# Performance work log

Hardware: AMD Instinct MI355X
Metric: run time of the kernel (lower is better)

Reference implementation:

```python
import jax, jax.numpy as jnp
import numpy as np

B, S, D, H, DH = 2, 4096, 768, 12, 64

def setup_inputs() -> dict:
    key = jax.random.key(0)
    kx, kq, kk, kv = jax.random.split(key, 4)
    x = jax.random.normal(kx, (B, S, D), dtype=jnp.float32)
    # per-head Q/K/V projection weights, stacked over heads: [H, d_in, d_out]
    Wq = jax.random.normal(kq, (H, D, DH), dtype=jnp.float32) * 0.02
    Wk = jax.random.normal(kk, (H, D, DH), dtype=jnp.float32) * 0.02
    Wv = jax.random.normal(kv, (H, D, DH), dtype=jnp.float32) * 0.02
    return {"x": x, "Wq": Wq, "Wk": Wk, "Wv": Wv}

def reference(x, Wq, Wk, Wv):
    b, s, _ = x.shape
    # per-head linear projections (qkv_bias=False), batched over heads
    q = jnp.einsum('bsd,hde->bhse', x, Wq)  # [B,H,S,DH]
    k = jnp.einsum('bsd,hde->bhse', x, Wk)
    v = jnp.einsum('bsd,hde->bhse', x, Wv)
    scale = 1.0 / jnp.sqrt(jnp.asarray(q.shape[-1], q.dtype))
    scores = jnp.einsum('bhqe,bhke->bhqk', q, k) * scale  # [B,H,S,S]
    causal_mask = jnp.triu(jnp.ones((s, s), dtype=bool), k=1)
    scores = jnp.where(causal_mask, -jnp.inf, scores)
    attn = jax.nn.softmax(scores, axis=-1)  # dropout p=0 -> identity
    ctx = jnp.einsum('bhqk,bhke->bhqe', attn, v)  # [B,H,S,DH]
    # concat heads on last dim (matches torch.cat of per-head outputs)
    return ctx.transpose(0, 2, 1, 3).reshape(b, s, -1)  # [B,S,H*DH]
```

## Files before the change

### kernel.cpp

```cpp
#include <hip/hip_runtime.h>
#include <hip/hip_bf16.h>
#include <stdint.h>

#define B_  2
#define S_  4096
#define D_  768
#define H_  12
#define DH_ 64
#define BS_ (B_*S_)

typedef __bf16 bf16x8 __attribute__((ext_vector_type(8)));
typedef short  svec8  __attribute__((ext_vector_type(8)));
typedef float  fvec4  __attribute__((ext_vector_type(4)));
typedef int    ivec4  __attribute__((ext_vector_type(4)));
typedef unsigned short ushort_t;

__device__ __forceinline__ ushort_t bfc(float f){
    return __builtin_bit_cast(ushort_t, (__bf16)f);
}

__device__ __forceinline__ unsigned cvt_pk_bf16(float lo, float hi){
    unsigned r;
    asm("v_cvt_pk_bf16_f32 %0, %1, %2" : "=v"(r) : "v"(lo), "v"(hi));
    return r;
}

__device__ __forceinline__ fvec4 mfma16(svec8 a, svec8 b, fvec4 c){
    return __builtin_amdgcn_mfma_f32_16x16x32_bf16(
        __builtin_bit_cast(bf16x8, a), __builtin_bit_cast(bf16x8, b), c, 0, 0, 0);
}

__global__ __launch_bounds__(256) void prep(
    const float* __restrict__ X,
    const float* __restrict__ Wq, const float* __restrict__ Wk, const float* __restrict__ Wv,
    ushort_t* __restrict__ Xb, ushort_t* __restrict__ Wsz)
{
    const int bid = blockIdx.x;
    if (bid < 3072) {
        size_t idx = ((size_t)bid * 256 + threadIdx.x) * 8;
        float4 d0 = *(const float4*)(X + idx);
        float4 d1 = *(const float4*)(X + idx + 4);
        bf16x8 pk;
        pk[0] = (__bf16)d0.x; pk[1] = (__bf16)d0.y;
        pk[2] = (__bf16)d0.z; pk[3] = (__bf16)d0.w;
        pk[4] = (__bf16)d1.x; pk[5] = (__bf16)d1.y;
        pk[6] = (__bf16)d1.z; pk[7] = (__bf16)d1.w;
        *(svec8*)(Xb + idx) = __builtin_bit_cast(svec8, pk);
    } else {
        const int v  = bid - 3072;
        const int wt = v % 3;
        const int hk = v / 3;
        const int h  = hk / 12, kt = hk % 12;
        const float* W  = (wt == 0) ? Wq : (wt == 1) ? Wk : Wv;
        const float* Wh = W + (size_t)h * (D_ * DH_) + (size_t)kt * 64 * DH_;
        ushort_t* dst = Wsz + (size_t)(hk * 3 + wt) * 4096;
        #pragma unroll
        for (int i = 0; i < 2; i++) {
            int a    = (threadIdx.x + 256 * i) * 8;
            int k5   = a >> 11;
            int nblk = (a >> 9) & 3;
            int n    = nblk * 16 + ((a >> 5) & 15);
            int q2   = (a >> 3) & 3;
            int k0   = k5 * 32 + q2 * 8;
            bf16x8 pk;
            #pragma unroll
            for (int j = 0; j < 8; j++) pk[j] = (__bf16)Wh[(k0 + j) * DH_ + n];
            *(svec8*)(dst + a) = __builtin_bit_cast(svec8, pk);
        }
    }
}

__global__ __launch_bounds__(256, 3) void qkv_proj(
    const ushort_t* __restrict__ Xb, const ushort_t* __restrict__ Wsz,
    ushort_t* __restrict__ Qb, ushort_t* __restrict__ Kb, ushort_t* __restrict__ Vg)
{
    const int m0 = blockIdx.x * 128;
    const int h  = blockIdx.y;

    __shared__ ushort_t smem[128 * 64 + 3 * 4096];
    ushort_t* Xs  = smem;
    ushort_t* Wts = smem + 128 * 64;
    ushort_t* XsT = smem;

    const int tid  = threadIdx.x;
    const int w    = tid >> 6;
    const int lane = tid & 63;
    const int quad = lane >> 4;
    const int l15  = lane & 15;
    const int lp8  = (l15 * 4 + quad) * 8;

    fvec4 acc[3][2][4];
    #pragma unroll
    for (int wt = 0; wt < 3; wt++)
        #pragma unroll
        for (int i = 0; i < 2; i++)
            #pragma unroll
            for (int j = 0; j < 4; j++) acc[wt][i][j] = (fvec4){0.f, 0.f, 0.f, 0.f};

    const ushort_t* xsrc = Xb + (size_t)m0 * D_;
    const ushort_t* wsrc = Wsz + (size_t)(h * 12) * 3 * 4096;

    int xr[4], xdu[4];
    #pragma unroll
    for (int i = 0; i < 4; i++) {
        int v = tid + 256 * i;
        int r = v >> 3, t = v & 7;
        xr[i]  = r * D_ + t * 8;
        xdu[i] = (((r >> 4) * 2 + (t >> 2)) * 64 + (r & 15) * 4 + (t & 3)) * 8;
    }

    svec8 xd[4];
    #pragma unroll
    for (int i = 0; i < 4; i++) xd[i] = *(const svec8*)(xsrc + xr[i]);

    for (int kt = 0; kt < 12; kt++) {
        const ushort_t* wp = wsrc + (size_t)kt * 3 * 4096;
        svec8 wd[6];
        #pragma unroll
        for (int j = 0; j < 6; j++)
            wd[j] = *(const svec8*)(wp + (tid + 256 * j) * 8);
        #pragma unroll
        for (int i = 0; i < 4; i++) *(svec8*)(Xs + xdu[i]) = xd[i];
        #pragma unroll
        for (int j = 0; j < 6; j++) *(svec8*)(Wts + (tid + 256 * j) * 8) = wd[j];
        __syncthreads();

        if (kt < 11) {
            #pragma unroll
            for (int i = 0; i < 4; i++)
                xd[i] = *(const svec8*)(xsrc + xr[i] + (kt + 1) * 64);
        }

        #pragma unroll
        for (int ks = 0; ks < 2; ks++) {
            svec8 a0 = *(const svec8*)(Xs + (4 * w + ks) * 512 + lp8);
            svec8 a1 = *(const svec8*)(Xs + (4 * w + 2 + ks) * 512 + lp8);
            #pragma unroll
            for (int wt = 0; wt < 3; wt++)
                #pragma unroll
                for (int ns = 0; ns < 4; ns++) {
                    svec8 b = *(const svec8*)(Wts + (wt * 8 + ks * 4 + ns) * 512 + lp8);
                    acc[wt][0][ns] = mfma16(a0, b, acc[wt][0][ns]);
                    acc[wt][1][ns] = mfma16(a1, b, acc[wt][1][ns]);
                }
        }
        __syncthreads();
    }

    const float qs = 0.18033688011112042f;
    #pragma unroll
    for (int ms = 0; ms < 2; ms++)
        #pragma unroll
        for (int ns = 0; ns < 4; ns++)
            #pragma unroll
            for (int r = 0; r < 4; r++) {
                int row = m0 + 32 * w + ms * 16 + quad * 4 + r;
                int col = h * DH_ + ns * 16 + l15;
                Qb[(size_t)row * D_ + col] = bfc(acc[0][ms][ns][r] * qs);
                Kb[(size_t)row * D_ + col] = bfc(acc[1][ms][ns][r]);
            }
    #pragma unroll
    for (int ms = 0; ms < 2; ms++)
        #pragma unroll
        for (int ns = 0; ns < 4; ns++)
            #pragma unroll
            for (int r = 0; r < 4; r++) {
                int sl = 32 * w + ms * 16 + quad * 4 + r;
                int e  = ns * 16 + l15;
                XsT[e * 136 + sl] = bfc(acc[2][ms][ns][r]);
            }
    __syncthreads();
    #pragma unroll
    for (int i = 0; i < 4; i++) {
        int v = tid + 256 * i;
        int e = v >> 4, s0 = (v & 15) * 8;
        svec8 d = *(const svec8*)(XsT + e * 136 + s0);
        *(svec8*)(Vg + (size_t)(h * DH_ + e) * BS_ + m0 + s0) = d;
    }
}

__global__ __launch_bounds__(256, 3) void attn(
    const ushort_t* __restrict__ Qb, const ushort_t* __restrict__ Kb,
    const ushort_t* __restrict__ Vg, float* __restrict__ Out)
{
    const int fid = blockIdx.x;
    const int c   = fid & 255;
    const int rnd = fid >> 8;
    const int t   = c & 31;
    const int u   = c >> 5;
    const int qtp = (rnd == 0) ? t : (rnd == 1) ? ((t + 16) & 31)
                                                : (t < 16 ? 30 - 2 * t : 63 - 2 * t);
    const int hb  = rnd * 8 + u;
    const int h   = hb % H_;
    const int b   = hb / H_;
    const int q0  = qtp * 128;
    const int qt2 = 2 * qtp + 1;

    const int tid  = threadIdx.x;
    const int w    = tid >> 6;
    const int lane = tid & 63;
    const int quad = lane >> 4;
    const int l15  = lane & 15;

    __shared__ ushort_t Ks[64 * 72];
    __shared__ ushort_t Vt[64 * 72];

    const size_t hboff = (size_t)b * S_ * D_ + (size_t)h * DH_;
    const ushort_t* Vh = Vg + (size_t)h * DH_ * BS_ + (size_t)b * S_;

    const int sr = tid >> 3;
    const int sc = (tid & 7) * 8;
    const int pr0 = (((sr      >> 2) & 1) << 5) | (((sr      >> 5) & 1) << 4) |
                    (((sr      >> 4) & 1) << 3) | (((sr      >> 3) & 1) << 2) | (sr & 3);
    const int sr1 = sr + 32;
    const int pr1 = (((sr1 >> 2) & 1) << 5) | (((sr1 >> 5) & 1) << 4) |
                    (((sr1 >> 4) & 1) << 3) | (((sr1 >> 3) & 1) << 2) | (sr1 & 3);

    svec8 aqA[2], aqB[2];
    {
        const ushort_t* qra = Qb + hboff + (size_t)(q0 + 16 * w + l15) * D_;
        aqA[0] = *(const svec8*)(qra + quad * 8);
        aqA[1] = *(const svec8*)(qra + 32 + quad * 8);
        const ushort_t* qrb = qra + (size_t)64 * D_;
        aqB[0] = *(const svec8*)(qrb + quad * 8);
        aqB[1] = *(const svec8*)(qrb + 32 + quad * 8);
    }

    float miA = -INFINITY, miB = -INFINITY;
    float lsA = 0.f, lsB = 0.f;
    fvec4 accA[4], accB[4];
    #pragma unroll
    for (int n = 0; n < 4; n++) {
        accA[n] = (fvec4){0.f, 0.f, 0.f, 0.f};
        accB[n] = (fvec4){0.f, 0.f, 0.f, 0.f};
    }

    const ushort_t* kp = Kb + hboff + (size_t)sr * D_ + sc;
    const ushort_t* vp = Vh + (size_t)sr * BS_ + sc;

    svec8 kd[2], vd[2];
    kd[0] = *(const svec8*)(kp);
    kd[1] = *(const svec8*)(kp + (size_t)32 * D_);
    vd[0] = *(const svec8*)(vp);
    vd[1] = *(const svec8*)(vp + (size_t)32 * BS_);
    kp += (size_t)64 * D_;
    vp += 64;
    *(svec8*)(Ks + pr0 * 72 + sc) = kd[0];
    *(svec8*)(Ks + pr1 * 72 + sc) = kd[1];
    *(svec8*)(Vt + sr  * 72 + sc) = vd[0];
    *(svec8*)(Vt + sr1 * 72 + sc) = vd[1];

    for (int kt = 0; kt <= qt2; ++kt) {
        __syncthreads();

        if (kt < qt2) {
            kd[0] = *(const svec8*)(kp);
            kd[1] = *(const svec8*)(kp + (size_t)32 * D_);
            vd[0] = *(const svec8*)(vp);
            vd[1] = *(const svec8*)(vp + (size_t)32 * BS_);
            kp += (size_t)64 * D_;
            vp += 64;
        }

        fvec4 stA[4], stB[4];
        #pragma unroll
        for (int n = 0; n < 4; n++) {
            stA[n] = (fvec4){0.f, 0.f, 0.f, 0.f};
            stB[n] = (fvec4){0.f, 0.f, 0.f, 0.f};
        }
        #pragma unroll
        for (int ks = 0; ks < 2; ks++)
            #pragma unroll
            for (int n = 0; n < 4; n++) {
                svec8 ka = *(const svec8*)(Ks + (n * 16 + l15) * 72 + ks * 32 + quad * 8);
                stA[n] = mfma16(ka, aqA[ks], stA[n]);
                stB[n] = mfma16(ka, aqB[ks], stB[n]);
            }

        if (kt == qt2 - 1) {
            #pragma unroll
            for (int n = 0; n < 4; n++)
                #pragma unroll
                for (int r = 0; r < 4; r++) {
                    int key = (n & 1) * 32 + quad * 8 + (n >> 1) * 4 + r;
                    int row = 16 * w + l15;
                    if (key > row) stA[n][r] = -INFINITY;
                }
        }
        if (kt == qt2) {
            #pragma unroll
            for (int n = 0; n < 4; n++)
                #pragma unroll
                for (int r = 0; r < 4; r++) {
                    stA[n][r] = -INFINITY;
                    int key = (n & 1) * 32 + quad * 8 + (n >> 1) * 4 + r;
                    int row = 16 * w + l15;
                    if (key > row) stB[n][r] = -INFINITY;
                }
        }

        float mxA, mxB;
        {
            float m1 = fmaxf(fmaxf(stA[0][0], stA[0][1]), stA[0][2]);
            m1 = fmaxf(fmaxf(m1, stA[0][3]), stA[1][0]);
            m1 = fmaxf(fmaxf(m1, stA[1][1]), stA[1][2]);
            m1 = fmaxf(m1, stA[1][3]);
            float m2 = fmaxf(fmaxf(stA[2][0], stA[2][1]), stA[2][2]);
            m2 = fmaxf(fmaxf(m2, stA[2][3]), stA[3][0]);
            m2 = fmaxf(fmaxf(m2, stA[3][1]), stA[3][2]);
            m2 = fmaxf(m2, stA[3][3]);
            mxA = fmaxf(m1, m2);
            mxA = fmaxf(mxA, __shfl_xor(mxA, 16));
            mxA = fmaxf(mxA, __shfl_xor(mxA, 32));
        }
        {
            float m1 = fmaxf(fmaxf(stB[0][0], stB[0][1]), stB[0][2]);
            m1 = fmaxf(fmaxf(m1, stB[0][3]), stB[1][0]);
            m1 = fmaxf(fmaxf(m1, stB[1][1]), stB[1][2]);
            m1 = fmaxf(m1, stB[1][3]);
            float m2 = fmaxf(fmaxf(stB[2][0], stB[2][1]), stB[2][2]);
            m2 = fmaxf(fmaxf(m2, stB[2][3]), stB[3][0]);
            m2 = fmaxf(fmaxf(m2, stB[3][1]), stB[3][2]);
            m2 = fmaxf(m2, stB[3][3]);
            mxB = fmaxf(m1, m2);
            mxB = fmaxf(mxB, __shfl_xor(mxB, 16));
            mxB = fmaxf(mxB, __shfl_xor(mxB, 32));
        }

        if (__any((mxA > miA) || (mxB > miB))) {
            float mnA = fmaxf(miA, mxA), mnB = fmaxf(miB, mxB);
            float aA = exp2f(miA - mnA), aB = exp2f(miB - mnB);
            miA = mnA; miB = mnB;
            lsA *= aA; lsB *= aB;
            #pragma unroll
            for (int r = 0; r < 4; r++) {
                float arA = __shfl(aA, quad * 16 + quad * 4 + r);
                float arB = __shfl(aB, quad * 16 + quad * 4 + r);
                #pragma unroll
                for (int n = 0; n < 4; n++) {
                    accA[n][r] *= arA;
                    accB[n][r] *= arB;
                }
            }
        }

        svec8 apA0, apA1, apB0, apB1;
        {
            ivec4 ai0, ai1;
            float ps[4];
            #pragma unroll
            for (int n = 0; n < 4; n++) {
                float p0 = exp2f(stA[n][0] - miA);
                float p1 = exp2f(stA[n][1] - miA);
                float p2 = exp2f(stA[n][2] - miA);
                float p3 = exp2f(stA[n][3] - miA);
                ps[n] = (p0 + p1) + (p2 + p3);
                unsigned d0 = cvt_pk_bf16(p0, p1);
                unsigned d1 = cvt_pk_bf16(p2, p3);
                if (n == 0)      { ai0[0] = (int)d0; ai0[1] = (int)d1; }
                else if (n == 1) { ai1[0] = (int)d0; ai1[1] = (int)d1; }
                else if (n == 2) { ai0[2] = (int)d0; ai0[3] = (int)d1; }
                else             { ai1[2] = (int)d0; ai1[3] = (int)d1; }
            }
            lsA += (ps[0] + ps[2]) + (ps[1] + ps[3]);
            apA0 = __builtin_bit_cast(svec8, ai0);
            apA1 = __builtin_bit_cast(svec8, ai1);
        }
        {
            ivec4 ai0, ai1;
            float ps[4];
            #pragma unroll
            for (int n = 0; n < 4; n++) {
                float p0 = exp2f(stB[n][0] - miB);
                float p1 = exp2f(stB[n][1] - miB);
                float p2 = exp2f(stB[n][2] - miB);
                float p3 = exp2f(stB[n][3] - miB);
                ps[n] = (p0 + p1) + (p2 + p3);
                unsigned d0 = cvt_pk_bf16(p0, p1);
                unsigned d1 = cvt_pk_bf16(p2, p3);
                if (n == 0)      { ai0[0] = (int)d0; ai0[1] = (int)d1; }
                else if (n == 1) { ai1[0] = (int)d0; ai1[1] = (int)d1; }
                else if (n == 2) { ai0[2] = (int)d0; ai0[3] = (int)d1; }
                else             { ai1[2] = (int)d0; ai1[3] = (int)d1; }
            }
            lsB += (ps[0] + ps[2]) + (ps[1] + ps[3]);
            apB0 = __builtin_bit_cast(svec8, ai0);
            apB1 = __builtin_bit_cast(svec8, ai1);
        }

        #pragma unroll
        for (int ks = 0; ks < 2; ks++) {
            svec8 apa = ks ? apA1 : apA0;
            svec8 apb = ks ? apB1 : apB0;
            #pragma unroll
            for (int n = 0; n < 4; n++) {
                svec8 bv = *(const svec8*)(Vt + (n * 16 + l15) * 72 + ks * 32 + quad * 8);
                accA[n] = mfma16(apa, bv, accA[n]);
                accB[n] = mfma16(apb, bv, accB[n]);
            }
        }

        __syncthreads();

        if (kt < qt2) {
            *(svec8*)(Ks + pr0 * 72 + sc) = kd[0];
            *(svec8*)(Ks + pr1 * 72 + sc) = kd[1];
            *(svec8*)(Vt + sr  * 72 + sc) = vd[0];
            *(svec8*)(Vt + sr1 * 72 + sc) = vd[1];
        }
    }

    float lsumA = lsA;
    lsumA += __shfl_xor(lsumA, 16);
    lsumA += __shfl_xor(lsumA, 32);
    float lsumB = lsB;
    lsumB += __shfl_xor(lsumB, 16);
    lsumB += __shfl_xor(lsumB, 32);
    #pragma unroll
    for (int r = 0; r < 4; r++) {
        float liA = __shfl(lsumA, quad * 16 + quad * 4 + r);
        float liB = __shfl(lsumB, quad * 16 + quad * 4 + r);
        int rowA = q0 + 16 * w + quad * 4 + r;
        #pragma unroll
        for (int n = 0; n < 4; n++) {
            int col = h * DH_ + n * 16 + l15;
            Out[((size_t)b * S_ + rowA) * D_ + col]      = accA[n][r] / liA;
            Out[((size_t)b * S_ + rowA + 64) * D_ + col] = accB[n][r] / liB;
        }
    }
}

extern "C" void kernel_launch(void* const* d_in, const int* in_sizes, int n_in,
                              void* d_out, int out_size, void* d_ws, size_t ws_size,
                              hipStream_t stream)
{
    const float* X  = (const float*)d_in[0];
    const float* Wq = (const float*)d_in[1];
    const float* Wk = (const float*)d_in[2];
    const float* Wv = (const float*)d_in[3];

    ushort_t* Qb = (ushort_t*)d_ws;
    ushort_t* Kb = Qb + (size_t)BS_ * D_;
    ushort_t* Vg = Kb + (size_t)BS_ * D_;

    ushort_t* Xb  = (ushort_t*)d_out;
    ushort_t* Wsz = Xb + (size_t)BS_ * D_;
    float* Out = (float*)d_out;

    prep<<<dim3(3072 + 432), dim3(256), 0, stream>>>(X, Wq, Wk, Wv, Xb, Wsz);
    qkv_proj<<<dim3(64, H_), dim3(256), 0, stream>>>(Xb, Wsz, Qb, Kb, Vg);
    attn<<<dim3(768), dim3(256), 0, stream>>>(Qb, Kb, Vg, Out);
}
```

Before: 248.6 us.

## Shrink attention blocks to 64-row tiles and read projection weights directly from global

The attention kernel now runs 128-thread blocks, each covering a 64-row query tile with two waves of 32 rows. Tiles are scheduled longest-first, and the paired-tile balancing scheme plus the two-step diagonal masking are replaced by a single diagonal step. This gives a finer grid for load balance and occupancy, at the cost of each K/V tile being reused by fewer query rows. The QKV projection also stops staging the pre-swizzled weights in LDS and loads MFMA B operands straight from global memory, which shrinks shared memory but adds global/L2 traffic inside the inner loop.

```diff
diff --git a/kernel.cpp b/kernel.cpp
--- a/kernel.cpp
+++ b/kernel.cpp
@@ -77,9 +77,8 @@
     const int m0 = blockIdx.x * 128;
     const int h  = blockIdx.y;
 
-    __shared__ ushort_t smem[128 * 64 + 3 * 4096];
+    __shared__ ushort_t smem[64 * 136];
     ushort_t* Xs  = smem;
-    ushort_t* Wts = smem + 128 * 64;
     ushort_t* XsT = smem;
 
     const int tid  = threadIdx.x;
@@ -98,7 +97,7 @@
             for (int j = 0; j < 4; j++) acc[wt][i][j] = (fvec4){0.f, 0.f, 0.f, 0.f};
 
     const ushort_t* xsrc = Xb + (size_t)m0 * D_;
-    const ushort_t* wsrc = Wsz + (size_t)(h * 12) * 3 * 4096;
+    const ushort_t* wsrc = Wsz + (size_t)(h * 12) * 3 * 4096 + lp8;
 
     int xr[4], xdu[4];
     #pragma unroll
@@ -114,15 +113,8 @@
     for (int i = 0; i < 4; i++) xd[i] = *(const svec8*)(xsrc + xr[i]);
 
     for (int kt = 0; kt < 12; kt++) {
-        const ushort_t* wp = wsrc + (size_t)kt * 3 * 4096;
-        svec8 wd[6];
-        #pragma unroll
-        for (int j = 0; j < 6; j++)
-            wd[j] = *(const svec8*)(wp + (tid + 256 * j) * 8);
         #pragma unroll
         for (int i = 0; i < 4; i++) *(svec8*)(Xs + xdu[i]) = xd[i];
-        #pragma unroll
-        for (int j = 0; j < 6; j++) *(svec8*)(Wts + (tid + 256 * j) * 8) = wd[j];
         __syncthreads();
 
         if (kt < 11) {
@@ -131,18 +123,23 @@
                 xd[i] = *(const svec8*)(xsrc + xr[i] + (kt + 1) * 64);
         }
 
+        const ushort_t* wp = wsrc + (size_t)kt * 3 * 4096;
         #pragma unroll
         for (int ks = 0; ks < 2; ks++) {
             svec8 a0 = *(const svec8*)(Xs + (4 * w + ks) * 512 + lp8);
             svec8 a1 = *(const svec8*)(Xs + (4 * w + 2 + ks) * 512 + lp8);
             #pragma unroll
-            for (int wt = 0; wt < 3; wt++)
+            for (int wt = 0; wt < 3; wt++) {
+                svec8 wb[4];
+                #pragma unroll
+                for (int ns = 0; ns < 4; ns++)
+                    wb[ns] = *(const svec8*)(wp + (wt * 8 + ks * 4 + ns) * 512);
                 #pragma unroll
                 for (int ns = 0; ns < 4; ns++) {
-                    svec8 b = *(const svec8*)(Wts + (wt * 8 + ks * 4 + ns) * 512 + lp8);
-                    acc[wt][0][ns] = mfma16(a0, b, acc[wt][0][ns]);
-                    acc[wt][1][ns] = mfma16(a1, b, acc[wt][1][ns]);
+                    acc[wt][0][ns] = mfma16(a0, wb[ns], acc[wt][0][ns]);
+                    acc[wt][1][ns] = mfma16(a1, wb[ns], acc[wt][1][ns]);
                 }
+            }
         }
         __syncthreads();
     }
@@ -179,22 +176,16 @@
     }
 }
 
-__global__ __launch_bounds__(256, 3) void attn(
+__global__ __launch_bounds__(128, 3) void attn(
     const ushort_t* __restrict__ Qb, const ushort_t* __restrict__ Kb,
     const ushort_t* __restrict__ Vg, float* __restrict__ Out)
 {
     const int fid = blockIdx.x;
-    const int c   = fid & 255;
-    const int rnd = fid >> 8;
-    const int t   = c & 31;
-    const int u   = c >> 5;
-    const int qtp = (rnd == 0) ? t : (rnd == 1) ? ((t + 16) & 31)
-                                                : (t < 16 ? 30 - 2 * t : 63 - 2 * t);
-    const int hb  = rnd * 8 + u;
-    const int h   = hb % H_;
-    const int b   = hb / H_;
-    const int q0  = qtp * 128;
-    const int qt2 = 2 * qtp + 1;
+    const int qt  = (S_ / 64 - 1) - fid / (H_ * B_);
+    const int r24 = fid % (H_ * B_);
+    const int h   = r24 % H_;
+    const int b   = r24 / H_;
+    const int q0 = qt * 64;
 
     const int tid  = threadIdx.x;
     const int w    = tid >> 6;
@@ -210,18 +201,20 @@
 
     const int sr = tid >> 3;
     const int sc = (tid & 7) * 8;
-    const int pr0 = (((sr      >> 2) & 1) << 5) | (((sr      >> 5) & 1) << 4) |
-                    (((sr      >> 4) & 1) << 3) | (((sr      >> 3) & 1) << 2) | (sr & 3);
-    const int sr1 = sr + 32;
-    const int pr1 = (((sr1 >> 2) & 1) << 5) | (((sr1 >> 5) & 1) << 4) |
-                    (((sr1 >> 4) & 1) << 3) | (((sr1 >> 3) & 1) << 2) | (sr1 & 3);
+    int pr[4];
+    #pragma unroll
+    for (int i = 0; i < 4; i++) {
+        int k = sr + 16 * i;
+        pr[i] = (((k >> 2) & 1) << 5) | (((k >> 5) & 1) << 4) |
+                (((k >> 4) & 1) << 3) | (((k >> 3) & 1) << 2) | (k & 3);
+    }
 
     svec8 aqA[2], aqB[2];
     {
-        const ushort_t* qra = Qb + hboff + (size_t)(q0 + 16 * w + l15) * D_;
+        const ushort_t* qra = Qb + hboff + (size_t)(q0 + 32 * w + l15) * D_;
         aqA[0] = *(const svec8*)(qra + quad * 8);
         aqA[1] = *(const svec8*)(qra + 32 + quad * 8);
-        const ushort_t* qrb = qra + (size_t)64 * D_;
+        const ushort_t* qrb = qra + (size_t)16 * D_;
         aqB[0] = *(const svec8*)(qrb + quad * 8);
         aqB[1] = *(const svec8*)(qrb + 32 + quad * 8);
     }
@@ -238,26 +231,29 @@
     const ushort_t* kp = Kb + hboff + (size_t)sr * D_ + sc;
     const ushort_t* vp = Vh + (size_t)sr * BS_ + sc;
 
-    svec8 kd[2], vd[2];
-    kd[0] = *(const svec8*)(kp);
-    kd[1] = *(const svec8*)(kp + (size_t)32 * D_);
-    vd[0] = *(const svec8*)(vp);
-    vd[1] = *(const svec8*)(vp + (size_t)32 * BS_);
+    svec8 kd[4], vd[4];
+    #pragma unroll
+    for (int i = 0; i < 4; i++) {
+        kd[i] = *(const svec8*)(kp + (size_t)(16 * i) * D_);
+        vd[i] = *(const svec8*)(vp + (size_t)(16 * i) * BS_);
+    }
     kp += (size_t)64 * D_;
     vp += 64;
-    *(svec8*)(Ks + pr0 * 72 + sc) = kd[0];
-    *(svec8*)(Ks + pr1 * 72 + sc) = kd[1];
-    *(svec8*)(Vt + sr  * 72 + sc) = vd[0];
-    *(svec8*)(Vt + sr1 * 72 + sc) = vd[1];
-
-    for (int kt = 0; kt <= qt2; ++kt) {
+    #pragma unroll
+    for (int i = 0; i < 4; i++) {
+        *(svec8*)(Ks + pr[i] * 72 + sc) = kd[i];
+        *(svec8*)(Vt + (sr + 16 * i) * 72 + sc) = vd[i];
+    }
+
+    for (int kt = 0; kt <= qt; ++kt) {
         __syncthreads();
 
-        if (kt < qt2) {
-            kd[0] = *(const svec8*)(kp);
-            kd[1] = *(const svec8*)(kp + (size_t)32 * D_);
-            vd[0] = *(const svec8*)(vp);
-            vd[1] = *(const svec8*)(vp + (size_t)32 * BS_);
+        if (kt < qt) {
+            #pragma unroll
+            for (int i = 0; i < 4; i++) {
+                kd[i] = *(const svec8*)(kp + (size_t)(16 * i) * D_);
+                vd[i] = *(const svec8*)(vp + (size_t)(16 * i) * BS_);
+            }
             kp += (size_t)64 * D_;
             vp += 64;
         }
@@ -277,25 +273,15 @@
                 stB[n] = mfma16(ka, aqB[ks], stB[n]);
             }
 
-        if (kt == qt2 - 1) {
+        if (kt == qt) {
             #pragma unroll
             for (int n = 0; n < 4; n++)
                 #pragma unroll
                 for (int r = 0; r < 4; r++) {
-                    int key = (n & 1) * 32 + quad * 8 + (n >> 1) * 4 + r;
-                    int row = 16 * w + l15;
-                    if (key > row) stA[n][r] = -INFINITY;
-                }
-        }
-        if (kt == qt2) {
-            #pragma unroll
-            for (int n = 0; n < 4; n++)
-                #pragma unroll
-                for (int r = 0; r < 4; r++) {
-                    stA[n][r] = -INFINITY;
-                    int key = (n & 1) * 32 + quad * 8 + (n >> 1) * 4 + r;
-                    int row = 16 * w + l15;
-                    if (key > row) stB[n][r] = -INFINITY;
+                    int key  = (n & 1) * 32 + quad * 8 + (n >> 1) * 4 + r;
+                    int rowA = 32 * w + l15;
+                    if (key > rowA)      stA[n][r] = -INFINITY;
+                    if (key > rowA + 16) stB[n][r] = -INFINITY;
                 }
         }
 
@@ -402,11 +388,12 @@
 
         __syncthreads();
 
-        if (kt < qt2) {
-            *(svec8*)(Ks + pr0 * 72 + sc) = kd[0];
-            *(svec8*)(Ks + pr1 * 72 + sc) = kd[1];
-            *(svec8*)(Vt + sr  * 72 + sc) = vd[0];
-            *(svec8*)(Vt + sr1 * 72 + sc) = vd[1];
+        if (kt < qt) {
+            #pragma unroll
+            for (int i = 0; i < 4; i++) {
+                *(svec8*)(Ks + pr[i] * 72 + sc) = kd[i];
+                *(svec8*)(Vt + (sr + 16 * i) * 72 + sc) = vd[i];
+            }
         }
     }
 
@@ -420,12 +407,12 @@
     for (int r = 0; r < 4; r++) {
         float liA = __shfl(lsumA, quad * 16 + quad * 4 + r);
         float liB = __shfl(lsumB, quad * 16 + quad * 4 + r);
-        int rowA = q0 + 16 * w + quad * 4 + r;
+        int rowA = q0 + 32 * w + quad * 4 + r;
         #pragma unroll
         for (int n = 0; n < 4; n++) {
             int col = h * DH_ + n * 16 + l15;
             Out[((size_t)b * S_ + rowA) * D_ + col]      = accA[n][r] / liA;
-            Out[((size_t)b * S_ + rowA + 64) * D_ + col] = accB[n][r] / liB;
+            Out[((size_t)b * S_ + rowA + 16) * D_ + col] = accB[n][r] / liB;
         }
     }
 }
@@ -449,5 +436,5 @@
 
     prep<<<dim3(3072 + 432), dim3(256), 0, stream>>>(X, Wq, Wk, Wv, Xb, Wsz);
     qkv_proj<<<dim3(64, H_), dim3(256), 0, stream>>>(Xb, Wsz, Qb, Kb, Vg);
-    attn<<<dim3(768), dim3(256), 0, stream>>>(Qb, Kb, Vg, Out);
-}
+    attn<<<dim3((S_ / 64) * H_ * B_), dim3(128), 0, stream>>>(Qb, Kb, Vg, Out);
+}
```

Result: slower. 271.6 us (+9.2%).
